# Kernel tuning notes

Hardware: AMD Instinct MI355X
Metric: run time of the kernel (lower is better)

Reference implementation:

```python
import jax, jax.numpy as jnp
import numpy as np

# --- static configuration (mirrors init_kwargs) ---
L = 16        # latent_size
HL = 512      # hypernet_layer_size
D = 64        # decoder_layer_size
NDEC = 2      # decoder_n_layers
B, G = 128, 100  # batch, grid (pressure levels)
LOGP_MEAN, LOGP_STD = 0.0, 3.0
T_MEAN, T_STD = 1500.0, 500.0

# decoder layer structure generated by the hypernet
WEIGHT_SIZES = [(1, D)] + [(D, D)] * NDEC + [(D, 1)]
BIAS_SIZES = [1] + [D] * NDEC + [1]
OUT_SIZE = sum(a * b for a, b in WEIGHT_SIZES) + sum(BIAS_SIZES)  # 8450


def setup_inputs() -> dict:
    key = jax.random.key(0)
    ks = jax.random.split(key, 8)
    def init(k, shape, fan_in):
        return (jax.random.normal(k, shape, jnp.float32) / np.float32(np.sqrt(fan_in)))
    return {
        "z": jax.random.normal(ks[0], (B, L), jnp.float32),
        "log_P": jax.random.normal(ks[1], (B, G), jnp.float32) * 2.0,
        # hypernet MLP params: L -> HL -> HL -> HL -> OUT_SIZE
        "hW0": init(ks[2], (L, HL), L), "hb0": jnp.zeros((HL,), jnp.float32),
        "hW1": init(ks[3], (HL, HL), HL), "hb1": jnp.zeros((HL,), jnp.float32),
        "hW2": init(ks[4], (HL, HL), HL), "hb2": jnp.zeros((HL,), jnp.float32),
        "hWo": init(ks[5], (HL, OUT_SIZE), HL), "hbo": jnp.zeros((OUT_SIZE,), jnp.float32),
    }


def reference(z, log_P, hW0, hb0, hW1, hb1, hW2, hb2, hWo, hbo):
    Bsz, Gsz = log_P.shape
    R = Bsz * Gsz  # flattened rows
    # broadcast latent over the pressure grid: (B, L) -> (R, L)
    z_flat = jnp.broadcast_to(z[:, None, :], (Bsz, Gsz, z.shape[-1])).reshape(R, -1)
    # normalize pressure -> decoder input, shape (R, 1)
    x = (log_P.reshape(R, 1) - LOGP_MEAN) / LOGP_STD
    # hypernet MLP (leaky_relu, slope 0.01 like torch default)
    h = jax.nn.leaky_relu(z_flat @ hW0 + hb0)
    h = jax.nn.leaky_relu(h @ hW1 + hb1)
    h = jax.nn.leaky_relu(h @ hW2 + hb2)
    wab = h @ hWo + hbo  # (R, OUT_SIZE): per-row decoder weights+biases
    # per-row decoder: chain of batched GEMVs with siren activation
    off = 0
    n_layers = len(WEIGHT_SIZES)
    for i, ((di, do), bs) in enumerate(zip(WEIGHT_SIZES, BIAS_SIZES)):
        n = di * do
        w = wab[:, off:off + n].reshape(R, di, do)
        b = wab[:, off + n:off + n + bs]  # broadcasts against (R, do)
        off += n + bs
        x = jnp.einsum('bi,bij->bj', x, w) + b
        if i == 0:
            x = x * 30.0  # siren first-layer omega_0
        if i < n_layers - 1:
            x = jnp.sin(x)  # siren activation; last layer is Identity
    T_pred = x.reshape(Bsz, Gsz)
    # undo temperature normalization
    return T_pred * T_STD + T_MEAN
```

## Files before the change

kernel.cpp:

```cpp
#include <hip/hip_runtime.h>

#define WSTRIDE 8704
#define GSTR 65

__device__ __forceinline__ float lrelu(float x) { return x > 0.0f ? x : 0.01f * x; }

__global__ __launch_bounds__(128) void h0T_kernel(const float* __restrict__ z,
                                                  const float* __restrict__ W,
                                                  const float* __restrict__ bias,
                                                  float* __restrict__ h0T) {
    int j = blockIdx.x;
    int b = threadIdx.x;
    float zr[16];
    *(float4*)&zr[0]  = *(const float4*)&z[b * 16 + 0];
    *(float4*)&zr[4]  = *(const float4*)&z[b * 16 + 4];
    *(float4*)&zr[8]  = *(const float4*)&z[b * 16 + 8];
    *(float4*)&zr[12] = *(const float4*)&z[b * 16 + 12];
    float acc = bias[j];
#pragma unroll
    for (int l = 0; l < 16; ++l) acc = fmaf(zr[l], W[l * 512 + j], acc);
    h0T[j * 128 + b] = lrelu(acc);
}

__global__ __launch_bounds__(256) void gemmT_kernel(const float* __restrict__ At,
                                                    const float* __restrict__ W,
                                                    const float* __restrict__ bias,
                                                    float* __restrict__ OT) {
    __shared__ __align__(16) float As[512][4];
    __shared__ float red[4][64][5];
    int jt = blockIdx.x & 7;
    int bt = blockIdx.x >> 3;
    int tid = threadIdx.x;
    int lane = tid & 63;
    int wid  = __builtin_amdgcn_readfirstlane(tid >> 6);
    int b0 = bt * 4;
#pragma unroll
    for (int r = 0; r < 4; ++r) {
        int p = r * 256 + tid;
        int k = p >> 1, q = p & 1;
        *(float2*)&As[k][q * 2] = *(const float2*)&At[k * 128 + b0 + q * 2];
    }
    __syncthreads();
    int j = jt * 64 + lane;
    float acc[4] = {};
    int k0 = wid * 128;
#pragma unroll 8
    for (int kk = 0; kk < 128; ++kk) {
        int k = k0 + kk;
        float4 a = *(const float4*)&As[k][0];
        float w = W[k * 512 + j];
        acc[0] = fmaf(a.x, w, acc[0]);
        acc[1] = fmaf(a.y, w, acc[1]);
        acc[2] = fmaf(a.z, w, acc[2]);
        acc[3] = fmaf(a.w, w, acc[3]);
    }
#pragma unroll
    for (int i = 0; i < 4; ++i) red[wid][lane][i] = acc[i];
    __syncthreads();
    int jj = tid >> 2;
    int bb = tid & 3;
    float s = red[0][jj][bb] + red[1][jj][bb] + red[2][jj][bb] + red[3][jj][bb];
    int jg = jt * 64 + jj;
    OT[jg * 128 + b0 + bb] = lrelu(s + bias[jg]);
}

__global__ __launch_bounds__(256) void wabT_kernel(const float* __restrict__ At,
                                                   const float* __restrict__ W,
                                                   const float* __restrict__ bias,
                                                   float* __restrict__ wab) {
    __shared__ __align__(16) float As[512][16];
    __shared__ float red[4][64][33];
    int tid = threadIdx.x;
    if (blockIdx.x == 528) {
        int b = tid & 127;
        int jc = 8448 + (tid >> 7);
        float a0 = 0.f, a1 = 0.f, a2 = 0.f, a3 = 0.f;
#pragma unroll 4
        for (int k4 = 0; k4 < 128; ++k4) {
            a0 = fmaf(At[(k4*4+0) * 128 + b], W[(k4*4+0) * 8450 + jc], a0);
            a1 = fmaf(At[(k4*4+1) * 128 + b], W[(k4*4+1) * 8450 + jc], a1);
            a2 = fmaf(At[(k4*4+2) * 128 + b], W[(k4*4+2) * 8450 + jc], a2);
            a3 = fmaf(At[(k4*4+3) * 128 + b], W[(k4*4+3) * 8450 + jc], a3);
        }
        wab[b * WSTRIDE + jc] = a0 + a1 + a2 + a3 + bias[jc];
        return;
    }
    int v = (blockIdx.x & 7) * 66 + (blockIdx.x >> 3);
    int jt = v >> 3;
    int bt = v & 7;
    int lane = tid & 63;
    int wid  = __builtin_amdgcn_readfirstlane(tid >> 6);
    int b0 = bt * 16;
#pragma unroll
    for (int r = 0; r < 16; ++r) {
        int p = r * 256 + tid;
        int k = p >> 3, q = p & 7;
        *(float2*)&As[k][q * 2] = *(const float2*)&At[k * 128 + b0 + q * 2];
    }
    __syncthreads();
    int j0 = jt * 128 + lane * 2;
    float acc[16][2] = {};
    int k0 = wid * 128;
#pragma unroll 4
    for (int kk = 0; kk < 128; ++kk) {
        int k = k0 + kk;
        float4 a0 = *(const float4*)&As[k][0];
        float4 a1 = *(const float4*)&As[k][4];
        float4 a2 = *(const float4*)&As[k][8];
        float4 a3 = *(const float4*)&As[k][12];
        float2 w = *(const float2*)&W[k * 8450 + j0];
        float av[16] = {a0.x,a0.y,a0.z,a0.w, a1.x,a1.y,a1.z,a1.w,
                        a2.x,a2.y,a2.z,a2.w, a3.x,a3.y,a3.z,a3.w};
#pragma unroll
        for (int bb = 0; bb < 16; ++bb) {
            acc[bb][0] = fmaf(av[bb], w.x, acc[bb][0]);
            acc[bb][1] = fmaf(av[bb], w.y, acc[bb][1]);
        }
    }
#pragma unroll
    for (int bb = 0; bb < 16; ++bb) {
        red[wid][lane][bb * 2 + 0] = acc[bb][0];
        red[wid][lane][bb * 2 + 1] = acc[bb][1];
    }
    __syncthreads();
    int jj = tid >> 1;
    int bh = tid & 1;
    int lane_r = jj >> 1;
    int jl = jj & 1;
    int jg = jt * 128 + jj;
    float bj = bias[jg];
#pragma unroll
    for (int bq = 0; bq < 8; ++bq) {
        int bb = bh * 8 + bq;
        int idx = bb * 2 + jl;
        float s = red[0][lane_r][idx] + red[1][lane_r][idx]
                + red[2][lane_r][idx] + red[3][lane_r][idx];
        wab[(b0 + bb) * WSTRIDE + jg] = s + bj;
    }
}

__global__ __launch_bounds__(256) void decoder_kernel(const float* __restrict__ wab,
                                                      const float* __restrict__ logP,
                                                      float* __restrict__ out) {
    __shared__ __align__(16) float Wl[64 * 64];
    __shared__ float hX[64 * GSTR];
    __shared__ float hY[64 * GSTR];
    __shared__ float red[4][68];
    int b   = blockIdx.x >> 1;
    int gbl = blockIdx.x & 1;
    int tid = threadIdx.x;
    int lane = tid & 63;
    int wid  = __builtin_amdgcn_readfirstlane(tid >> 6);
    int jq = wid * 16;
    int g = gbl * 64 + lane;
    bool act = g < 100;
    const float* __restrict__ row = wab + b * WSTRIDE;
    float x0 = act ? logP[b * 100 + g] * (1.0f / 3.0f) : 0.0f;

    float c0 = row[64];
#pragma unroll
    for (int t = 0; t < 16; ++t)
        hX[(jq + t) * GSTR + lane] = __sinf(30.0f * fmaf(x0, row[jq + t], c0));
#pragma unroll
    for (int r = 0; r < 16; ++r) {
        int idx = r * 256 + tid;
        Wl[idx] = row[65 + idx];
    }
    __syncthreads();

    {
        float a[16];
#pragma unroll
        for (int t = 0; t < 16; ++t) a[t] = row[4161 + jq + t];
#pragma unroll 4
        for (int i = 0; i < 64; ++i) {
            float hi = hX[i * GSTR + lane];
            const float* wr = &Wl[i * 64 + jq];
            float4 w0 = *(const float4*)&wr[0];
            float4 w1 = *(const float4*)&wr[4];
            float4 w2 = *(const float4*)&wr[8];
            float4 w3 = *(const float4*)&wr[12];
            a[0]  = fmaf(hi, w0.x, a[0]);  a[1]  = fmaf(hi, w0.y, a[1]);
            a[2]  = fmaf(hi, w0.z, a[2]);  a[3]  = fmaf(hi, w0.w, a[3]);
            a[4]  = fmaf(hi, w1.x, a[4]);  a[5]  = fmaf(hi, w1.y, a[5]);
            a[6]  = fmaf(hi, w1.z, a[6]);  a[7]  = fmaf(hi, w1.w, a[7]);
            a[8]  = fmaf(hi, w2.x, a[8]);  a[9]  = fmaf(hi, w2.y, a[9]);
            a[10] = fmaf(hi, w2.z, a[10]); a[11] = fmaf(hi, w2.w, a[11]);
            a[12] = fmaf(hi, w3.x, a[12]); a[13] = fmaf(hi, w3.y, a[13]);
            a[14] = fmaf(hi, w3.z, a[14]); a[15] = fmaf(hi, w3.w, a[15]);
        }
#pragma unroll
        for (int t = 0; t < 16; ++t) hY[(jq + t) * GSTR + lane] = __sinf(a[t]);
    }
    __syncthreads();
#pragma unroll
    for (int r = 0; r < 16; ++r) {
        int idx = r * 256 + tid;
        Wl[idx] = row[4225 + idx];
    }
    __syncthreads();

    {
        float a[16];
#pragma unroll
        for (int t = 0; t < 16; ++t) a[t] = row[8321 + jq + t];
#pragma unroll 4
        for (int i = 0; i < 64; ++i) {
            float hi = hY[i * GSTR + lane];
            const float* wr = &Wl[i * 64 + jq];
            float4 w0 = *(const float4*)&wr[0];
            float4 w1 = *(const float4*)&wr[4];
            float4 w2 = *(const float4*)&wr[8];
            float4 w3 = *(const float4*)&wr[12];
            a[0]  = fmaf(hi, w0.x, a[0]);  a[1]  = fmaf(hi, w0.y, a[1]);
            a[2]  = fmaf(hi, w0.z, a[2]);  a[3]  = fmaf(hi, w0.w, a[3]);
            a[4]  = fmaf(hi, w1.x, a[4]);  a[5]  = fmaf(hi, w1.y, a[5]);
            a[6]  = fmaf(hi, w1.z, a[6]);  a[7]  = fmaf(hi, w1.w, a[7]);
            a[8]  = fmaf(hi, w2.x, a[8]);  a[9]  = fmaf(hi, w2.y, a[9]);
            a[10] = fmaf(hi, w2.z, a[10]); a[11] = fmaf(hi, w2.w, a[11]);
            a[12] = fmaf(hi, w3.x, a[12]); a[13] = fmaf(hi, w3.y, a[13]);
            a[14] = fmaf(hi, w3.z, a[14]); a[15] = fmaf(hi, w3.w, a[15]);
        }
#pragma unroll
        for (int t = 0; t < 16; ++t) hX[(jq + t) * GSTR + lane] = __sinf(a[t]);
    }
    __syncthreads();

    float p = 0.f;
#pragma unroll
    for (int t = 0; t < 16; ++t)
        p = fmaf(hX[(jq + t) * GSTR + lane], row[8385 + jq + t], p);
    red[wid][lane] = p;
    __syncthreads();
    if (wid == 0 && act) {
        float s = red[0][lane] + red[1][lane] + red[2][lane] + red[3][lane] + row[8449];
        out[b * 100 + g] = fmaf(s, 500.0f, 1500.0f);
    }
}

extern "C" void kernel_launch(void* const* d_in, const int* in_sizes, int n_in,
                              void* d_out, int out_size, void* d_ws, size_t ws_size,
                              hipStream_t stream) {
    const float* z    = (const float*)d_in[0];
    const float* logP = (const float*)d_in[1];
    const float* hW0  = (const float*)d_in[2];
    const float* hb0  = (const float*)d_in[3];
    const float* hW1  = (const float*)d_in[4];
    const float* hb1  = (const float*)d_in[5];
    const float* hW2  = (const float*)d_in[6];
    const float* hb2  = (const float*)d_in[7];
    const float* hWo  = (const float*)d_in[8];
    const float* hbo  = (const float*)d_in[9];
    float* out = (float*)d_out;

    float* wab = (float*)d_ws;
    float* h0T = wab + 128 * WSTRIDE;
    float* h1T = h0T + 512 * 128;
    float* h2T = h1T + 512 * 128;

    h0T_kernel<<<512, 128, 0, stream>>>(z, hW0, hb0, h0T);
    gemmT_kernel<<<256, 256, 0, stream>>>(h0T, hW1, hb1, h1T);
    gemmT_kernel<<<256, 256, 0, stream>>>(h1T, hW2, hb2, h2T);
    wabT_kernel<<<529, 256, 0, stream>>>(h2T, hWo, hbo, wab);
    decoder_kernel<<<256, 256, 0, stream>>>(wab, logP, out);
}
```

Before: 72.71 us.

## Split-K register-tiled output GEMM with partial buffers, shifted wab layout, global-read decoder

The big hypernet output GEMM now uses a 16x8 register tile per thread with split-K over two halves and four waves, software double-buffered loads, and writes eight partial-sum planes to workspace. A new add kernel reduces the partials, adds bias, and writes wab with a 3-float shift so the 64x64 decoder weight blocks are 16-byte aligned. The decoder then reads weights straight from global memory instead of staging them in LDS. The hidden-layer GEMMs move to 512 threads with an 8-way K split. The aim is more FMA reuse per load and more parallelism, at the cost of about 35 MB of extra partial-sum traffic and one extra launch.

```diff
diff --git a/kernel.cpp b/kernel.cpp
--- a/kernel.cpp
+++ b/kernel.cpp
@@ -1,7 +1,7 @@
 #include <hip/hip_runtime.h>
 
 #define WSTRIDE 8704
-#define GSTR 65
+#define PSZ (128 * WSTRIDE)
 
 __device__ __forceinline__ float lrelu(float x) { return x > 0.0f ? x : 0.01f * x; }
 
@@ -22,12 +22,12 @@
     h0T[j * 128 + b] = lrelu(acc);
 }
 
-__global__ __launch_bounds__(256) void gemmT_kernel(const float* __restrict__ At,
+__global__ __launch_bounds__(512) void gemmT_kernel(const float* __restrict__ At,
                                                     const float* __restrict__ W,
                                                     const float* __restrict__ bias,
                                                     float* __restrict__ OT) {
     __shared__ __align__(16) float As[512][4];
-    __shared__ float red[4][64][5];
+    __shared__ float red[8][64][5];
     int jt = blockIdx.x & 7;
     int bt = blockIdx.x >> 3;
     int tid = threadIdx.x;
@@ -35,17 +35,17 @@
     int wid  = __builtin_amdgcn_readfirstlane(tid >> 6);
     int b0 = bt * 4;
 #pragma unroll
-    for (int r = 0; r < 4; ++r) {
-        int p = r * 256 + tid;
+    for (int r = 0; r < 2; ++r) {
+        int p = r * 512 + tid;
         int k = p >> 1, q = p & 1;
         *(float2*)&As[k][q * 2] = *(const float2*)&At[k * 128 + b0 + q * 2];
     }
     __syncthreads();
     int j = jt * 64 + lane;
     float acc[4] = {};
-    int k0 = wid * 128;
+    int k0 = wid * 64;
 #pragma unroll 8
-    for (int kk = 0; kk < 128; ++kk) {
+    for (int kk = 0; kk < 64; ++kk) {
         int k = k0 + kk;
         float4 a = *(const float4*)&As[k][0];
         float w = W[k * 512 + j];
@@ -57,125 +57,175 @@
 #pragma unroll
     for (int i = 0; i < 4; ++i) red[wid][lane][i] = acc[i];
     __syncthreads();
-    int jj = tid >> 2;
-    int bb = tid & 3;
-    float s = red[0][jj][bb] + red[1][jj][bb] + red[2][jj][bb] + red[3][jj][bb];
-    int jg = jt * 64 + jj;
-    OT[jg * 128 + b0 + bb] = lrelu(s + bias[jg]);
+    if (tid < 256) {
+        int jj = tid >> 2;
+        int bb = tid & 3;
+        float s = 0.f;
+#pragma unroll
+        for (int w = 0; w < 8; ++w) s += red[w][jj][bb];
+        int jg = jt * 64 + jj;
+        OT[jg * 128 + b0 + bb] = lrelu(s + bias[jg]);
+    }
+}
+
+__device__ __forceinline__ void ldk(const float (*Asw)[16], const float* Wp, int kk,
+                                    float (&a)[16], float (&w)[8]) {
+    float4 t0 = *(const float4*)&Asw[kk][0];
+    float4 t1 = *(const float4*)&Asw[kk][4];
+    float4 t2 = *(const float4*)&Asw[kk][8];
+    float4 t3 = *(const float4*)&Asw[kk][12];
+    a[0]=t0.x; a[1]=t0.y; a[2]=t0.z; a[3]=t0.w;
+    a[4]=t1.x; a[5]=t1.y; a[6]=t1.z; a[7]=t1.w;
+    a[8]=t2.x; a[9]=t2.y; a[10]=t2.z; a[11]=t2.w;
+    a[12]=t3.x; a[13]=t3.y; a[14]=t3.z; a[15]=t3.w;
+    const float* wr = Wp + (size_t)kk * 8450;
+    float2 u0 = *(const float2*)&wr[0];
+    float2 u1 = *(const float2*)&wr[2];
+    float2 u2 = *(const float2*)&wr[4];
+    float2 u3 = *(const float2*)&wr[6];
+    w[0]=u0.x; w[1]=u0.y; w[2]=u1.x; w[3]=u1.y;
+    w[4]=u2.x; w[5]=u2.y; w[6]=u3.x; w[7]=u3.y;
+}
+__device__ __forceinline__ void fmak(const float (&a)[16], const float (&w)[8],
+                                     float (&acc)[16][8]) {
+#pragma unroll
+    for (int i = 0; i < 16; ++i)
+#pragma unroll
+        for (int j = 0; j < 8; ++j)
+            acc[i][j] = fmaf(a[i], w[j], acc[i][j]);
 }
 
 __global__ __launch_bounds__(256) void wabT_kernel(const float* __restrict__ At,
                                                    const float* __restrict__ W,
-                                                   const float* __restrict__ bias,
-                                                   float* __restrict__ wab) {
-    __shared__ __align__(16) float As[512][16];
-    __shared__ float red[4][64][33];
+                                                   float* __restrict__ parts) {
+    __shared__ __align__(16) float As[256][16];
     int tid = threadIdx.x;
-    if (blockIdx.x == 528) {
-        int b = tid & 127;
-        int jc = 8448 + (tid >> 7);
-        float a0 = 0.f, a1 = 0.f, a2 = 0.f, a3 = 0.f;
-#pragma unroll 4
-        for (int k4 = 0; k4 < 128; ++k4) {
-            a0 = fmaf(At[(k4*4+0) * 128 + b], W[(k4*4+0) * 8450 + jc], a0);
-            a1 = fmaf(At[(k4*4+1) * 128 + b], W[(k4*4+1) * 8450 + jc], a1);
-            a2 = fmaf(At[(k4*4+2) * 128 + b], W[(k4*4+2) * 8450 + jc], a2);
-            a3 = fmaf(At[(k4*4+3) * 128 + b], W[(k4*4+3) * 8450 + jc], a3);
-        }
-        wab[b * WSTRIDE + jc] = a0 + a1 + a2 + a3 + bias[jc];
-        return;
-    }
-    int v = (blockIdx.x & 7) * 66 + (blockIdx.x >> 3);
-    int jt = v >> 3;
-    int bt = v & 7;
     int lane = tid & 63;
-    int wid  = __builtin_amdgcn_readfirstlane(tid >> 6);
+    int wid = __builtin_amdgcn_readfirstlane(tid >> 6);
+    int jt, bt, kh;
+    bool tail = blockIdx.x >= 256;
+    if (!tail) {
+        int x = blockIdx.x & 7, w = blockIdx.x >> 3;
+        jt = x + 8 * (w >> 4);
+        bt = (w >> 1) & 7;
+        kh = w & 1;
+    } else {
+        int r = blockIdx.x - 256;
+        jt = 16; bt = r >> 1; kh = r & 1;
+    }
     int b0 = bt * 16;
-#pragma unroll
-    for (int r = 0; r < 16; ++r) {
+    int k0b = kh * 256;
+#pragma unroll
+    for (int r = 0; r < 4; ++r) {
         int p = r * 256 + tid;
-        int k = p >> 3, q = p & 7;
-        *(float2*)&As[k][q * 2] = *(const float2*)&At[k * 128 + b0 + q * 2];
-    }
-    __syncthreads();
-    int j0 = jt * 128 + lane * 2;
-    float acc[16][2] = {};
-    int k0 = wid * 128;
-#pragma unroll 4
-    for (int kk = 0; kk < 128; ++kk) {
-        int k = k0 + kk;
-        float4 a0 = *(const float4*)&As[k][0];
-        float4 a1 = *(const float4*)&As[k][4];
-        float4 a2 = *(const float4*)&As[k][8];
-        float4 a3 = *(const float4*)&As[k][12];
-        float2 w = *(const float2*)&W[k * 8450 + j0];
-        float av[16] = {a0.x,a0.y,a0.z,a0.w, a1.x,a1.y,a1.z,a1.w,
-                        a2.x,a2.y,a2.z,a2.w, a3.x,a3.y,a3.z,a3.w};
+        int k = p >> 2, q = p & 3;
+        *(float4*)&As[k][q * 4] = *(const float4*)&At[(k0b + k) * 128 + b0 + q * 4];
+    }
+    __syncthreads();
+    int kw = wid * 64;
+    int j0 = jt * 512 + lane * 8;
+    float acc[16][8];
+#pragma unroll
+    for (int i = 0; i < 16; ++i)
+#pragma unroll
+        for (int j = 0; j < 8; ++j) acc[i][j] = 0.0f;
+    const float (*Asw)[16] = (const float (*)[16])&As[kw];
+
+    if (!tail) {
+        const float* Wp = W + (size_t)(k0b + kw) * 8450 + j0;
+        float aA[16], wA[8], aB[16], wB[8];
+        ldk(Asw, Wp, 0, aA, wA);
+        ldk(Asw, Wp, 1, aB, wB);
+        for (int kk = 0; kk < 62; kk += 2) {
+            fmak(aA, wA, acc);
+            ldk(Asw, Wp, kk + 2, aA, wA);
+            fmak(aB, wB, acc);
+            if (kk + 3 < 64) ldk(Asw, Wp, kk + 3, aB, wB);
+        }
+        fmak(aA, wA, acc);
+        fmak(aB, wB, acc);
+        size_t pbase = (size_t)(kh * 4 + wid) * PSZ;
 #pragma unroll
         for (int bb = 0; bb < 16; ++bb) {
-            acc[bb][0] = fmaf(av[bb], w.x, acc[bb][0]);
-            acc[bb][1] = fmaf(av[bb], w.y, acc[bb][1]);
-        }
-    }
-#pragma unroll
-    for (int bb = 0; bb < 16; ++bb) {
-        red[wid][lane][bb * 2 + 0] = acc[bb][0];
-        red[wid][lane][bb * 2 + 1] = acc[bb][1];
-    }
-    __syncthreads();
-    int jj = tid >> 1;
-    int bh = tid & 1;
-    int lane_r = jj >> 1;
-    int jl = jj & 1;
-    int jg = jt * 128 + jj;
-    float bj = bias[jg];
-#pragma unroll
-    for (int bq = 0; bq < 8; ++bq) {
-        int bb = bh * 8 + bq;
-        int idx = bb * 2 + jl;
-        float s = red[0][lane_r][idx] + red[1][lane_r][idx]
-                + red[2][lane_r][idx] + red[3][lane_r][idx];
-        wab[(b0 + bb) * WSTRIDE + jg] = s + bj;
+            float* d = parts + pbase + (size_t)(b0 + bb) * WSTRIDE + j0;
+            *(float4*)&d[0] = make_float4(acc[bb][0], acc[bb][1], acc[bb][2], acc[bb][3]);
+            *(float4*)&d[4] = make_float4(acc[bb][4], acc[bb][5], acc[bb][6], acc[bb][7]);
+        }
+    } else if (j0 < 8450) {
+        for (int kk = 0; kk < 64; ++kk) {
+            const float* wr = W + (size_t)(k0b + kw + kk) * 8450;
+            float w[8];
+#pragma unroll
+            for (int e = 0; e < 8; ++e) {
+                int j = j0 + e;
+                w[e] = wr[j < 8450 ? j : 8449];
+            }
+            float a[16];
+#pragma unroll
+            for (int i = 0; i < 16; ++i) a[i] = Asw[kk][i];
+            fmak(a, w, acc);
+        }
+        size_t pbase = (size_t)(kh * 4 + wid) * PSZ;
+#pragma unroll
+        for (int bb = 0; bb < 16; ++bb)
+#pragma unroll
+            for (int e = 0; e < 8; ++e)
+                if (j0 + e < 8450)
+                    parts[pbase + (size_t)(b0 + bb) * WSTRIDE + j0 + e] = acc[bb][e];
+    }
+}
+
+__global__ __launch_bounds__(256) void add_kernel(const float* __restrict__ parts,
+                                                  const float* __restrict__ bias,
+                                                  float* __restrict__ wab) {
+    int q = blockIdx.x * 256 + threadIdx.x;
+    if (q >= 2113) return;
+    int b = blockIdx.y;
+    int j0 = q * 4;
+    size_t off = (size_t)b * WSTRIDE + j0;
+    float s[4] = {0.f, 0.f, 0.f, 0.f};
+#pragma unroll
+    for (int p = 0; p < 8; ++p) {
+        float4 v = *(const float4*)&parts[(size_t)p * PSZ + off];
+        s[0] += v.x; s[1] += v.y; s[2] += v.z; s[3] += v.w;
+    }
+    float* drow = wab + (size_t)b * WSTRIDE;
+#pragma unroll
+    for (int e = 0; e < 4; ++e) {
+        int j = j0 + e;
+        if (j < 8450)
+            drow[j + (j >= 65 ? 3 : 0)] = s[e] + bias[j];
     }
 }
 
 __global__ __launch_bounds__(256) void decoder_kernel(const float* __restrict__ wab,
                                                       const float* __restrict__ logP,
                                                       float* __restrict__ out) {
-    __shared__ __align__(16) float Wl[64 * 64];
-    __shared__ float hX[64 * GSTR];
-    __shared__ float hY[64 * GSTR];
+    __shared__ float hX[64 * 65];
+    __shared__ float hY[64 * 65];
     __shared__ float red[4][68];
-    int b   = blockIdx.x >> 1;
-    int gbl = blockIdx.x & 1;
+    int b  = blockIdx.x >> 1;
+    int gh = blockIdx.x & 1;
     int tid = threadIdx.x;
     int lane = tid & 63;
-    int wid  = __builtin_amdgcn_readfirstlane(tid >> 6);
-    int jq = wid * 16;
-    int g = gbl * 64 + lane;
+    int jq = (tid >> 6) * 16;
+    int g = gh * 64 + lane;
     bool act = g < 100;
-    const float* __restrict__ row = wab + b * WSTRIDE;
+    const float* __restrict__ row = wab + (size_t)b * WSTRIDE;
     float x0 = act ? logP[b * 100 + g] * (1.0f / 3.0f) : 0.0f;
-
     float c0 = row[64];
 #pragma unroll
     for (int t = 0; t < 16; ++t)
-        hX[(jq + t) * GSTR + lane] = __sinf(30.0f * fmaf(x0, row[jq + t], c0));
-#pragma unroll
-    for (int r = 0; r < 16; ++r) {
-        int idx = r * 256 + tid;
-        Wl[idx] = row[65 + idx];
-    }
-    __syncthreads();
-
+        hX[(jq + t) * 65 + lane] = __sinf(30.0f * fmaf(x0, row[jq + t], c0));
+    __syncthreads();
     {
         float a[16];
 #pragma unroll
-        for (int t = 0; t < 16; ++t) a[t] = row[4161 + jq + t];
+        for (int t = 0; t < 16; ++t) a[t] = row[4164 + jq + t];
 #pragma unroll 4
         for (int i = 0; i < 64; ++i) {
-            float hi = hX[i * GSTR + lane];
-            const float* wr = &Wl[i * 64 + jq];
+            float hi = hX[i * 65 + lane];
+            const float* wr = row + 68 + i * 64 + jq;
             float4 w0 = *(const float4*)&wr[0];
             float4 w1 = *(const float4*)&wr[4];
             float4 w2 = *(const float4*)&wr[8];
@@ -190,24 +240,17 @@
             a[14] = fmaf(hi, w3.z, a[14]); a[15] = fmaf(hi, w3.w, a[15]);
         }
 #pragma unroll
-        for (int t = 0; t < 16; ++t) hY[(jq + t) * GSTR + lane] = __sinf(a[t]);
-    }
-    __syncthreads();
-#pragma unroll
-    for (int r = 0; r < 16; ++r) {
-        int idx = r * 256 + tid;
-        Wl[idx] = row[4225 + idx];
-    }
-    __syncthreads();
-
+        for (int t = 0; t < 16; ++t) hY[(jq + t) * 65 + lane] = __sinf(a[t]);
+    }
+    __syncthreads();
     {
         float a[16];
 #pragma unroll
-        for (int t = 0; t < 16; ++t) a[t] = row[8321 + jq + t];
+        for (int t = 0; t < 16; ++t) a[t] = row[8324 + jq + t];
 #pragma unroll 4
         for (int i = 0; i < 64; ++i) {
-            float hi = hY[i * GSTR + lane];
-            const float* wr = &Wl[i * 64 + jq];
+            float hi = hY[i * 65 + lane];
+            const float* wr = row + 4228 + i * 64 + jq;
             float4 w0 = *(const float4*)&wr[0];
             float4 w1 = *(const float4*)&wr[4];
             float4 w2 = *(const float4*)&wr[8];
@@ -222,18 +265,17 @@
             a[14] = fmaf(hi, w3.z, a[14]); a[15] = fmaf(hi, w3.w, a[15]);
         }
 #pragma unroll
-        for (int t = 0; t < 16; ++t) hX[(jq + t) * GSTR + lane] = __sinf(a[t]);
-    }
-    __syncthreads();
-
+        for (int t = 0; t < 16; ++t) hX[(jq + t) * 65 + lane] = __sinf(a[t]);
+    }
+    __syncthreads();
     float p = 0.f;
 #pragma unroll
     for (int t = 0; t < 16; ++t)
-        p = fmaf(hX[(jq + t) * GSTR + lane], row[8385 + jq + t], p);
-    red[wid][lane] = p;
-    __syncthreads();
-    if (wid == 0 && act) {
-        float s = red[0][lane] + red[1][lane] + red[2][lane] + red[3][lane] + row[8449];
+        p = fmaf(hX[(jq + t) * 65 + lane], row[8388 + jq + t], p);
+    red[tid >> 6][lane] = p;
+    __syncthreads();
+    if (tid < 64 && act) {
+        float s = red[0][lane] + red[1][lane] + red[2][lane] + red[3][lane] + row[8452];
         out[b * 100 + g] = fmaf(s, 500.0f, 1500.0f);
     }
 }
@@ -253,14 +295,16 @@
     const float* hbo  = (const float*)d_in[9];
     float* out = (float*)d_out;
 
-    float* wab = (float*)d_ws;
-    float* h0T = wab + 128 * WSTRIDE;
-    float* h1T = h0T + 512 * 128;
-    float* h2T = h1T + 512 * 128;
+    float* parts = (float*)d_ws;
+    float* wabF  = parts + 8 * (size_t)PSZ;
+    float* h0T   = wabF + PSZ;
+    float* h1T   = h0T + 512 * 128;
+    float* h2T   = h1T + 512 * 128;
 
     h0T_kernel<<<512, 128, 0, stream>>>(z, hW0, hb0, h0T);
-    gemmT_kernel<<<256, 256, 0, stream>>>(h0T, hW1, hb1, h1T);
-    gemmT_kernel<<<256, 256, 0, stream>>>(h1T, hW2, hb2, h2T);
-    wabT_kernel<<<529, 256, 0, stream>>>(h2T, hWo, hbo, wab);
-    decoder_kernel<<<256, 256, 0, stream>>>(wab, logP, out);
-}
+    gemmT_kernel<<<256, 512, 0, stream>>>(h0T, hW1, hb1, h1T);
+    gemmT_kernel<<<256, 512, 0, stream>>>(h1T, hW2, hb2, h2T);
+    wabT_kernel<<<272, 256, 0, stream>>>(h2T, hWo, parts);
+    add_kernel<<<dim3(9, 128), 256, 0, stream>>>(parts, hbo, wabF);
+    decoder_kernel<<<256, 256, 0, stream>>>(wabF, logP, out);
+}
```

New measurement: 105.1 us. +44.6%, slower.
